# Kernel optimization log

Measured on AMD Instinct MI355X. Metric: run time of the kernel, lower is better.

The kernel has to match this reference:

```python
import jax, jax.numpy as jnp
import numpy as np

B, T, DIM = 2, 2048, 2048
N_HEADS, N_KV_HEADS = 16, 4
HEAD_DIM = DIM // N_HEADS  # 128
N_REP = N_HEADS // N_KV_HEADS  # 4
ROPE_THETA = 10000.0


def setup_inputs() -> dict:
    key = jax.random.key(0)
    ks = jax.random.split(key, 5)
    x = jax.random.normal(ks[0], (B, T, DIM), dtype=jnp.float32)
    # RoPE tables (equivalent to complex freqs_cis = exp(i * t * inv_freq))
    inv_freq = 1.0 / (ROPE_THETA ** (np.arange(0, HEAD_DIM, 2, dtype=np.float32) / HEAD_DIM))
    t = np.arange(T, dtype=np.float32)
    ang = np.outer(t, inv_freq)  # (T, HEAD_DIM//2)
    freqs_cos = jnp.asarray(np.cos(ang), dtype=jnp.float32)
    freqs_sin = jnp.asarray(np.sin(ang), dtype=jnp.float32)
    s = 0.02
    wq = jax.random.normal(ks[1], (DIM, N_HEADS * HEAD_DIM), dtype=jnp.float32) * s
    wk = jax.random.normal(ks[2], (DIM, N_KV_HEADS * HEAD_DIM), dtype=jnp.float32) * s
    wv = jax.random.normal(ks[3], (DIM, N_KV_HEADS * HEAD_DIM), dtype=jnp.float32) * s
    wo = jax.random.normal(ks[4], (N_HEADS * HEAD_DIM, DIM), dtype=jnp.float32) * s
    return {"x": x, "freqs_cos": freqs_cos, "freqs_sin": freqs_sin,
            "wq": wq, "wk": wk, "wv": wv, "wo": wo}


def _apply_rope(t, cos, sin):
    # t: (B, H, T, hd); cos/sin: (T, hd//2); interleaved pairs like view_as_complex
    tr = t[..., 0::2]
    ti = t[..., 1::2]
    c = cos[None, None, :, :]
    s = sin[None, None, :, :]
    out_r = tr * c - ti * s
    out_i = tr * s + ti * c
    return jnp.stack([out_r, out_i], axis=-1).reshape(t.shape)


def reference(x, freqs_cos, freqs_sin, wq, wk, wv, wo):
    Bb, Tt, C = x.shape
    q = (x @ wq).reshape(Bb, Tt, N_HEADS, HEAD_DIM).transpose(0, 2, 1, 3)      # (B,H,T,hd)
    k = (x @ wk).reshape(Bb, Tt, N_KV_HEADS, HEAD_DIM).transpose(0, 2, 1, 3)   # (B,KV,T,hd)
    v = (x @ wv).reshape(Bb, Tt, N_KV_HEADS, HEAD_DIM).transpose(0, 2, 1, 3)
    q = _apply_rope(q, freqs_cos[:Tt], freqs_sin[:Tt])
    k = _apply_rope(k, freqs_cos[:Tt], freqs_sin[:Tt])
    # GQA repeat_kv
    k = jnp.repeat(k, N_REP, axis=1)  # (B,H,T,hd)
    v = jnp.repeat(v, N_REP, axis=1)
    scale = 1.0 / jnp.sqrt(jnp.float32(HEAD_DIM))
    scores = jnp.einsum("bhqd,bhkd->bhqk", q, k) * scale
    causal = jnp.tril(jnp.ones((Tt, Tt), dtype=bool))
    scores = jnp.where(causal[None, None], scores, jnp.float32(-jnp.inf))
    attn = jax.nn.softmax(scores, axis=-1)
    out = jnp.einsum("bhqk,bhkd->bhqd", attn, v)          # (B,H,T,hd)
    out = out.transpose(0, 2, 1, 3).reshape(Bb, Tt, C)
    return out @ wo
```

## Files before the change

### kernel.cpp

```cpp
#include <hip/hip_runtime.h>
#include <hip/hip_bf16.h>

#define SEQT 2048
#define NH 16
#define HD 128

typedef __bf16 bf16;
typedef __bf16 bf16x4 __attribute__((ext_vector_type(4)));
typedef __bf16 bf16x8 __attribute__((ext_vector_type(8)));
typedef float f32x4 __attribute__((ext_vector_type(4)));

__device__ inline void glds16(const bf16* g, bf16* l) {
  __builtin_amdgcn_global_load_lds(
      (const __attribute__((address_space(1))) unsigned int*)g,
      (__attribute__((address_space(3))) unsigned int*)l, 16, 0, 0);
}

__global__ __launch_bounds__(256) void k_convert(const float* __restrict__ in,
                                                 bf16* __restrict__ out, int n8) {
  int i = blockIdx.x * 256 + threadIdx.x;
  if (i >= n8) return;
  const float4* p = (const float4*)in + (size_t)i * 2;
  float4 a = p[0], b = p[1];
  bf16x8 o;
  o[0] = (bf16)a.x; o[1] = (bf16)a.y; o[2] = (bf16)a.z; o[3] = (bf16)a.w;
  o[4] = (bf16)b.x; o[5] = (bf16)b.y; o[6] = (bf16)b.z; o[7] = (bf16)b.w;
  *((bf16x8*)out + i) = o;
}

__global__ __launch_bounds__(256) void k_transpose(const float* __restrict__ in,
                                                   bf16* __restrict__ out, int R, int C) {
  __shared__ float tile[32][33];
  int c0 = blockIdx.x * 32, r0 = blockIdx.y * 32;
  int tx = threadIdx.x, ty = threadIdx.y;
#pragma unroll
  for (int i = 0; i < 4; i++)
    tile[ty + i * 8][tx] = in[(size_t)(r0 + ty + i * 8) * C + c0 + tx];
  __syncthreads();
#pragma unroll
  for (int i = 0; i < 4; i++) {
    int r = ty + i * 8;
    out[(size_t)(c0 + r) * R + r0 + tx] = (bf16)tile[tx][r];
  }
}

template <typename OutT>
__global__ __launch_bounds__(256) void k_gemm(const bf16* __restrict__ A,
                                              const bf16* __restrict__ Bt,
                                              OutT* __restrict__ C,
                                              int M, int N, int K, int ldc) {
  __shared__ bf16 Al[128 * 32];
  __shared__ bf16 Bl[128 * 32];
  int tid = threadIdx.x;
  int m0 = blockIdx.y * 128, n0 = blockIdx.x * 128;
  int wid = tid >> 6, lane = tid & 63;
  int wr = (wid >> 1) * 64, wc = (wid & 1) * 64;
  int lr = lane & 15, lk = (lane >> 4) * 8;
  f32x4 acc[4][4] = {};

  for (int k0 = 0; k0 < K; k0 += 32) {
#pragma unroll
    for (int i = 0; i < 2; i++) {
      int idx = i * 256 + tid;
      int r = idx >> 2, kc = (idx & 3) * 8;
      glds16(A + (size_t)(m0 + r) * K + k0 + kc, Al + idx * 8);
      glds16(Bt + (size_t)(n0 + r) * K + k0 + kc, Bl + idx * 8);
    }
    __syncthreads();
    bf16x8 af[4], bfr[4];
#pragma unroll
    for (int mi = 0; mi < 4; mi++) af[mi] = *(const bf16x8*)&Al[(wr + mi * 16 + lr) * 32 + lk];
#pragma unroll
    for (int ni = 0; ni < 4; ni++) bfr[ni] = *(const bf16x8*)&Bl[(wc + ni * 16 + lr) * 32 + lk];
#pragma unroll
    for (int mi = 0; mi < 4; mi++)
#pragma unroll
      for (int ni = 0; ni < 4; ni++)
        acc[mi][ni] = __builtin_amdgcn_mfma_f32_16x16x32_bf16(af[mi], bfr[ni], acc[mi][ni], 0, 0, 0);
    __syncthreads();
  }

  int rbase = m0 + wr + ((lane >> 4) << 2);
#pragma unroll
  for (int mi = 0; mi < 4; mi++)
#pragma unroll
    for (int ni = 0; ni < 4; ni++)
#pragma unroll
      for (int r = 0; r < 4; r++) {
        int row = rbase + mi * 16 + r;
        int col = n0 + wc + ni * 16 + lr;
        C[(size_t)row * ldc + col] = (OutT)acc[mi][ni][r];
      }
}

__global__ __launch_bounds__(256) void k_rope(bf16* __restrict__ qkv,
                                              const float* __restrict__ fcos,
                                              const float* __restrict__ fsin) {
  int gid = blockIdx.x * 256 + threadIdx.x;
  int row = gid / 1280;
  int p = gid % 1280;
  int head = p >> 6;
  int dp = p & 63;
  int t = row & (SEQT - 1);
  int colbase = head < NH ? head * HD : NH * HD + (head - NH) * HD;
  bf16* ptr = qkv + (size_t)row * 3072 + colbase + dp * 2;
  float a = (float)ptr[0], b = (float)ptr[1];
  float c = fcos[t * 64 + dp], s = fsin[t * 64 + dp];
  ptr[0] = (bf16)(a * c - b * s);
  ptr[1] = (bf16)(a * s + b * c);
}

__global__ __launch_bounds__(256, 2) void k_attn(const bf16* __restrict__ qkv,
                                                 bf16* __restrict__ attout) {
  __shared__ bf16 Kl[2][64 * 128];
  __shared__ bf16 Vt[128][72];
  __shared__ bf16 Pl[4][16][72];
  int bid = blockIdx.x;
  int qt = 31 - (bid >> 5);
  int bh = bid & 31;
  int b = bh >> 4, h = bh & 15, kvh = h >> 2;
  int tid = threadIdx.x, wid = tid >> 6, lane = tid & 63;
  int lr = lane & 15;
  int g = lane >> 4;
  int g4 = g * 4, g8 = g * 8, g16 = g * 16;
  int swz = (lr & 7) << 4;
  int q0 = qt * 64;
  const float scale = 0.08838834764831845f;

  const bf16* kgbase = qkv + (size_t)b * SEQT * 3072 + 2048 + kvh * HD;
  const bf16* vgbase = kgbase + 512;

  bf16x8 qf[4];
  {
    const bf16* qb = qkv + (size_t)(b * SEQT + q0 + wid * 16 + lr) * 3072 + h * HD;
#pragma unroll
    for (int db = 0; db < 4; db++) qf[db] = *(const bf16x8*)(qb + db * 32 + g8);
  }
  float mrun[4] = {-INFINITY, -INFINITY, -INFINITY, -INFINITY};
  float lpart[4] = {0.f, 0.f, 0.f, 0.f};
  f32x4 o[8] = {};
  int nkt = qt + 1;
  int qg0 = q0 + wid * 16 + g4;

  int kq4 = (wid * 4 + g) * 4;
  int dc = lr * 8;
  int xr = (lr & 7) << 3;
  int kvw = kq4 ^ xr;

  bf16x8 vr0, vr1, vr2, vr3;

#pragma unroll
  for (int r = 0; r < 4; r++) {
    int ci = r * 256 + tid;
    int row = ci >> 4;
    int sl = (ci & 15) ^ (row & 7);
    glds16(kgbase + (size_t)row * 3072 + sl * 8, &Kl[0][ci * 8]);
  }
  {
    const bf16* vrow = vgbase + (size_t)kq4 * 3072 + dc;
    vr0 = *(const bf16x8*)(vrow);
    vr1 = *(const bf16x8*)(vrow + 3072);
    vr2 = *(const bf16x8*)(vrow + 6144);
    vr3 = *(const bf16x8*)(vrow + 9216);
  }

  for (int kt = 0; kt < nkt; kt++) {
    int cur = kt & 1;
    asm volatile("s_waitcnt vmcnt(0)" ::: "memory");

#pragma unroll
    for (int j = 0; j < 8; j++) {
      bf16x4 w;
      w[0] = vr0[j]; w[1] = vr1[j]; w[2] = vr2[j]; w[3] = vr3[j];
      *(bf16x4*)&Vt[dc + j][kvw] = w;
    }

    if (kt + 1 < nkt) {
      int kv1 = (kt + 1) * 64;
      bf16* kdst = &Kl[(kt + 1) & 1][0];
#pragma unroll
      for (int r = 0; r < 4; r++) {
        int ci = r * 256 + tid;
        int row = ci >> 4;
        int sl = (ci & 15) ^ (row & 7);
        glds16(kgbase + (size_t)(kv1 + row) * 3072 + sl * 8, kdst + ci * 8);
      }
      const bf16* vrow = vgbase + (size_t)(kv1 + kq4) * 3072 + dc;
      vr0 = *(const bf16x8*)(vrow);
      vr1 = *(const bf16x8*)(vrow + 3072);
      vr2 = *(const bf16x8*)(vrow + 6144);
      vr3 = *(const bf16x8*)(vrow + 9216);
    }

    asm volatile("s_waitcnt lgkmcnt(0)" ::: "memory");
    __builtin_amdgcn_sched_barrier(0);
    __builtin_amdgcn_s_barrier();
    __builtin_amdgcn_sched_barrier(0);

    int kv0 = kt * 64;
    f32x4 s[4] = {};
    __builtin_amdgcn_s_setprio(1);
#pragma unroll
    for (int cb = 0; cb < 4; cb++) {
      const char* krow = (const char*)(&Kl[cur][0] + (cb * 16 + lr) * 128);
#pragma unroll
      for (int db = 0; db < 4; db++) {
        bf16x8 kf = *(const bf16x8*)(krow + ((db * 64 + g16) ^ swz));
        s[cb] = __builtin_amdgcn_mfma_f32_16x16x32_bf16(qf[db], kf, s[cb], 0, 0, 0);
      }
    }
    __builtin_amdgcn_s_setprio(0);

    float pv[4][4];
    float pmax[4] = {-INFINITY, -INFINITY, -INFINITY, -INFINITY};
#pragma unroll
    for (int cb = 0; cb < 4; cb++) {
      int kvg = kv0 + cb * 16 + lr;
#pragma unroll
      for (int r = 0; r < 4; r++) {
        float v = s[cb][r] * scale;
        if (kvg > qg0 + r) v = -INFINITY;
        pv[cb][r] = v;
        pmax[r] = fmaxf(pmax[r], v);
      }
    }
#pragma unroll
    for (int mk = 1; mk <= 8; mk <<= 1)
#pragma unroll
      for (int r = 0; r < 4; r++) pmax[r] = fmaxf(pmax[r], __shfl_xor(pmax[r], mk));
    float grow = fmaxf(fmaxf(pmax[0] - mrun[0], pmax[1] - mrun[1]),
                       fmaxf(pmax[2] - mrun[2], pmax[3] - mrun[3]));
    if (!__all(grow <= 8.0f)) {
#pragma unroll
      for (int r = 0; r < 4; r++) {
        float mnew = fmaxf(mrun[r], pmax[r]);
        float alpha = __expf(mrun[r] - mnew);
        mrun[r] = mnew;
        lpart[r] *= alpha;
#pragma unroll
        for (int df = 0; df < 8; df++) o[df][r] *= alpha;
      }
    }
#pragma unroll
    for (int r = 0; r < 4; r++) {
      float rs = 0.f;
#pragma unroll
      for (int cb = 0; cb < 4; cb++) {
        float e = __expf(pv[cb][r] - mrun[r]);
        pv[cb][r] = e;
        rs += e;
      }
      lpart[r] += rs;
    }

#pragma unroll
    for (int cb = 0; cb < 4; cb++)
#pragma unroll
      for (int r = 0; r < 4; r++)
        Pl[wid][g4 + r][cb * 16 + lr] = (bf16)pv[cb][r];

    __builtin_amdgcn_s_setprio(1);
#pragma unroll
    for (int kb = 0; kb < 2; kb++) {
      bf16x8 pa = *(const bf16x8*)&Pl[wid][lr][kb * 32 + g8];
#pragma unroll
      for (int df = 0; df < 8; df++) {
        int d = df * 16 + lr;
        int xv = ((d >> 3) & 7) << 3;
        bf16x8 vb = *(const bf16x8*)&Vt[d][(kb * 32 + g8) ^ xv];
        o[df] = __builtin_amdgcn_mfma_f32_16x16x32_bf16(pa, vb, o[df], 0, 0, 0);
      }
    }
    __builtin_amdgcn_s_setprio(0);
    __builtin_amdgcn_sched_barrier(0);
    __builtin_amdgcn_s_barrier();
    __builtin_amdgcn_sched_barrier(0);
  }

#pragma unroll
  for (int mk = 1; mk <= 8; mk <<= 1)
#pragma unroll
    for (int r = 0; r < 4; r++) lpart[r] += __shfl_xor(lpart[r], mk);
#pragma unroll
  for (int r = 0; r < 4; r++) {
    float inv = 1.f / lpart[r];
    int qg = q0 + wid * 16 + g4 + r;
    bf16* ob = attout + (size_t)(b * SEQT + qg) * 2048 + h * HD;
#pragma unroll
    for (int df = 0; df < 8; df++)
      ob[df * 16 + lr] = (bf16)(o[df][r] * inv);
  }
}

extern "C" void kernel_launch(void* const* d_in, const int* in_sizes, int n_in,
                              void* d_out, int out_size, void* d_ws, size_t ws_size,
                              hipStream_t stream) {
  const float* x    = (const float*)d_in[0];
  const float* fcos = (const float*)d_in[1];
  const float* fsin = (const float*)d_in[2];
  const float* wq   = (const float*)d_in[3];
  const float* wk   = (const float*)d_in[4];
  const float* wv   = (const float*)d_in[5];
  const float* wo   = (const float*)d_in[6];
  float* out = (float*)d_out;

  char* ws = (char*)d_ws;
  bf16* XB  = (bf16*)ws;
  bf16* W   = (bf16*)(ws + 16777216);
  bf16* QKV = (bf16*)(ws + 16777216 + 12582912);

  dim3 tb(32, 8);
  k_transpose<<<dim3(64, 64), tb, 0, stream>>>(wq, W, 2048, 2048);
  k_transpose<<<dim3(16, 64), tb, 0, stream>>>(wk, W + 2048 * 2048, 2048, 512);
  k_transpose<<<dim3(16, 64), tb, 0, stream>>>(wv, W + 2560 * 2048, 2048, 512);
  k_convert<<<4096, 256, 0, stream>>>(x, XB, 1048576);
  k_gemm<bf16><<<dim3(24, 32), 256, 0, stream>>>(XB, W, QKV, 4096, 3072, 2048, 3072);
  k_rope<<<20480, 256, 0, stream>>>(QKV, fcos, fsin);
  k_attn<<<1024, 256, 0, stream>>>(QKV, XB);
  k_transpose<<<dim3(64, 64), tb, 0, stream>>>(wo, W, 2048, 2048);
  k_gemm<float><<<dim3(16, 32), 256, 0, stream>>>(XB, W, out, 4096, 2048, 2048, 2048);
}
```

Measured before the change: 242.2 us.

## Restructure attention to 32x32 MFMA with 128-row query tiles and register-resident P

```diff
diff --git a/kernel.cpp b/kernel.cpp
--- a/kernel.cpp
+++ b/kernel.cpp
@@ -9,11 +9,18 @@
 typedef __bf16 bf16x4 __attribute__((ext_vector_type(4)));
 typedef __bf16 bf16x8 __attribute__((ext_vector_type(8)));
 typedef float f32x4 __attribute__((ext_vector_type(4)));
+typedef float f32x16 __attribute__((ext_vector_type(16)));
 
 __device__ inline void glds16(const bf16* g, bf16* l) {
   __builtin_amdgcn_global_load_lds(
       (const __attribute__((address_space(1))) unsigned int*)g,
       (__attribute__((address_space(3))) unsigned int*)l, 16, 0, 0);
+}
+
+__device__ inline unsigned int cvtpk(float a, float b) {
+  unsigned int d;
+  asm("v_cvt_pk_bf16_f32 %0, %1, %2" : "=v"(d) : "v"(a), "v"(b));
+  return d;
 }
 
 __global__ __launch_bounds__(256) void k_convert(const float* __restrict__ in,
@@ -114,34 +121,34 @@
                                                  bf16* __restrict__ attout) {
   __shared__ bf16 Kl[2][64 * 128];
   __shared__ bf16 Vt[128][72];
-  __shared__ bf16 Pl[4][16][72];
+  __shared__ float Atab[4][32];
   int bid = blockIdx.x;
-  int qt = 31 - (bid >> 5);
+  int qt = 15 - (bid >> 5);
   int bh = bid & 31;
   int b = bh >> 4, h = bh & 15, kvh = h >> 2;
   int tid = threadIdx.x, wid = tid >> 6, lane = tid & 63;
-  int lr = lane & 15;
-  int g = lane >> 4;
-  int g4 = g * 4, g8 = g * 8, g16 = g * 16;
-  int swz = (lr & 7) << 4;
-  int q0 = qt * 64;
-  const float scale = 0.08838834764831845f;
+  int li = lane & 31, hi = lane >> 5;
+  int q0 = qt * 128;
+  int qmin = q0 + wid * 32, qmax = qmin + 31;
+  int qlane = qmin + li;
+  const float C1 = 0.12751744979927212f;
 
   const bf16* kgbase = qkv + (size_t)b * SEQT * 3072 + 2048 + kvh * HD;
   const bf16* vgbase = kgbase + 512;
 
-  bf16x8 qf[4];
+  bf16x8 qf[8];
   {
-    const bf16* qb = qkv + (size_t)(b * SEQT + q0 + wid * 16 + lr) * 3072 + h * HD;
-#pragma unroll
-    for (int db = 0; db < 4; db++) qf[db] = *(const bf16x8*)(qb + db * 32 + g8);
-  }
-  float mrun[4] = {-INFINITY, -INFINITY, -INFINITY, -INFINITY};
-  float lpart[4] = {0.f, 0.f, 0.f, 0.f};
-  f32x4 o[8] = {};
-  int nkt = qt + 1;
-  int qg0 = q0 + wid * 16 + g4;
-
+    const bf16* qb = qkv + (size_t)(b * SEQT + qlane) * 3072 + h * HD + hi * 8;
+#pragma unroll
+    for (int ks = 0; ks < 8; ks++) qf[ks] = *(const bf16x8*)(qb + ks * 16);
+  }
+
+  float mrun = -INFINITY, lpart = 0.f;
+  f32x16 o0 = {}, o1 = {}, o2 = {}, o3 = {};
+  int nkt = 2 * qt + 2;
+
+  int g = (lane >> 4) & 3;
+  int lr = lane & 15;
   int kq4 = (wid * 4 + g) * 4;
   int dc = lr * 8;
   int xr = (lr & 7) << 3;
@@ -153,7 +160,7 @@
   for (int r = 0; r < 4; r++) {
     int ci = r * 256 + tid;
     int row = ci >> 4;
-    int sl = (ci & 15) ^ (row & 7);
+    int sl = (ci & 15) ^ (row & 15);
     glds16(kgbase + (size_t)row * 3072 + sl * 8, &Kl[0][ci * 8]);
   }
   {
@@ -166,6 +173,7 @@
 
   for (int kt = 0; kt < nkt; kt++) {
     int cur = kt & 1;
+    int kv0 = kt * 64;
     asm volatile("s_waitcnt vmcnt(0)" ::: "memory");
 
 #pragma unroll
@@ -176,13 +184,13 @@
     }
 
     if (kt + 1 < nkt) {
-      int kv1 = (kt + 1) * 64;
-      bf16* kdst = &Kl[(kt + 1) & 1][0];
+      int kv1 = kv0 + 64;
+      bf16* kdst = &Kl[cur ^ 1][0];
 #pragma unroll
       for (int r = 0; r < 4; r++) {
         int ci = r * 256 + tid;
         int row = ci >> 4;
-        int sl = (ci & 15) ^ (row & 7);
+        int sl = (ci & 15) ^ (row & 15);
         glds16(kgbase + (size_t)(kv1 + row) * 3072 + sl * 8, kdst + ci * 8);
       }
       const bf16* vrow = vgbase + (size_t)(kv1 + kq4) * 3072 + dc;
@@ -197,98 +205,145 @@
     __builtin_amdgcn_s_barrier();
     __builtin_amdgcn_sched_barrier(0);
 
-    int kv0 = kt * 64;
-    f32x4 s[4] = {};
-    __builtin_amdgcn_s_setprio(1);
-#pragma unroll
-    for (int cb = 0; cb < 4; cb++) {
-      const char* krow = (const char*)(&Kl[cur][0] + (cb * 16 + lr) * 128);
-#pragma unroll
-      for (int db = 0; db < 4; db++) {
-        bf16x8 kf = *(const bf16x8*)(krow + ((db * 64 + g16) ^ swz));
-        s[cb] = __builtin_amdgcn_mfma_f32_16x16x32_bf16(qf[db], kf, s[cb], 0, 0, 0);
-      }
+    if (kv0 <= qmax) {
+      f32x16 s0 = {}, s1 = {};
+      const char* kb0 = (const char*)&Kl[cur][0] + li * 256;
+      __builtin_amdgcn_s_setprio(1);
+#pragma unroll
+      for (int ks = 0; ks < 8; ks++) {
+        int off = ((ks * 2 + hi) ^ (li & 15)) << 4;
+        bf16x8 kf0 = *(const bf16x8*)(kb0 + off);
+        bf16x8 kf1 = *(const bf16x8*)(kb0 + 8192 + off);
+        s0 = __builtin_amdgcn_mfma_f32_32x32x16_bf16(kf0, qf[ks], s0, 0, 0, 0);
+        s1 = __builtin_amdgcn_mfma_f32_32x32x16_bf16(kf1, qf[ks], s1, 0, 0, 0);
+      }
+      __builtin_amdgcn_s_setprio(0);
+
+      if (kv0 + 63 > qmin) {
+        int base0 = kv0 + 4 * hi - qlane;
+#pragma unroll
+        for (int r = 0; r < 16; r++) {
+          int off = (r & 3) + 8 * (r >> 2);
+          if (base0 + off > 0) s0[r] = -INFINITY;
+          if (base0 + 32 + off > 0) s1[r] = -INFINITY;
+        }
+      }
+
+      float pm = s0[0];
+#pragma unroll
+      for (int r = 1; r < 16; r++) pm = fmaxf(pm, s0[r]);
+#pragma unroll
+      for (int r = 0; r < 16; r++) pm = fmaxf(pm, s1[r]);
+      pm = fmaxf(pm, __shfl_xor(pm, 32));
+
+      if (!__all(pm - mrun <= 62.0f)) {
+        float mnew = fmaxf(mrun, pm);
+        float alpha = exp2f((mrun - mnew) * C1);
+        mrun = mnew;
+        lpart *= alpha;
+        Atab[wid][li] = alpha;
+        asm volatile("s_waitcnt lgkmcnt(0)" ::: "memory");
+        f32x4 a0 = *(const f32x4*)&Atab[wid][4 * hi];
+        f32x4 a1 = *(const f32x4*)&Atab[wid][4 * hi + 8];
+        f32x4 a2 = *(const f32x4*)&Atab[wid][4 * hi + 16];
+        f32x4 a3 = *(const f32x4*)&Atab[wid][4 * hi + 24];
+#define RESC_RR(rr, av)                                            \
+  _Pragma("unroll") for (int i = 0; i < 4; i++) {                  \
+    float f = av[i];                                               \
+    o0[rr * 4 + i] *= f; o1[rr * 4 + i] *= f;                      \
+    o2[rr * 4 + i] *= f; o3[rr * 4 + i] *= f;                      \
+  }
+        RESC_RR(0, a0) RESC_RR(1, a1) RESC_RR(2, a2) RESC_RR(3, a3)
+#undef RESC_RR
+      }
+
+      float mC = mrun * C1;
+      float rs = 0.f;
+#pragma unroll
+      for (int r = 0; r < 16; r++) {
+        float p = exp2f(fmaf(s0[r], C1, -mC));
+        s0[r] = p; rs += p;
+      }
+#pragma unroll
+      for (int r = 0; r < 16; r++) {
+        float p = exp2f(fmaf(s1[r], C1, -mC));
+        s1[r] = p; rs += p;
+      }
+      lpart += rs;
+
+      union U4 { unsigned int u[4]; bf16x8 v; };
+      U4 pa0, pa1, pa2, pa3;
+      {
+        unsigned int e0 = cvtpk(s0[0], s0[1]), e1 = cvtpk(s0[2], s0[3]);
+        unsigned int e2 = cvtpk(s0[4], s0[5]), e3 = cvtpk(s0[6], s0[7]);
+        unsigned int e4 = cvtpk(s0[8], s0[9]), e5 = cvtpk(s0[10], s0[11]);
+        unsigned int e6 = cvtpk(s0[12], s0[13]), e7 = cvtpk(s0[14], s0[15]);
+        unsigned int t0 = __shfl_xor(e0, 32), t1 = __shfl_xor(e1, 32);
+        unsigned int t2 = __shfl_xor(e2, 32), t3 = __shfl_xor(e3, 32);
+        unsigned int t4 = __shfl_xor(e4, 32), t5 = __shfl_xor(e5, 32);
+        unsigned int t6 = __shfl_xor(e6, 32), t7 = __shfl_xor(e7, 32);
+        pa0.u[0] = hi ? t2 : e0;  pa0.u[1] = hi ? t3 : e1;
+        pa0.u[2] = hi ? e2 : t0;  pa0.u[3] = hi ? e3 : t1;
+        pa1.u[0] = hi ? t6 : e4;  pa1.u[1] = hi ? t7 : e5;
+        pa1.u[2] = hi ? e6 : t4;  pa1.u[3] = hi ? e7 : t5;
+        unsigned int f0 = cvtpk(s1[0], s1[1]), f1 = cvtpk(s1[2], s1[3]);
+        unsigned int f2 = cvtpk(s1[4], s1[5]), f3 = cvtpk(s1[6], s1[7]);
+        unsigned int f4 = cvtpk(s1[8], s1[9]), f5 = cvtpk(s1[10], s1[11]);
+        unsigned int f6 = cvtpk(s1[12], s1[13]), f7 = cvtpk(s1[14], s1[15]);
+        unsigned int u0 = __shfl_xor(f0, 32), u1 = __shfl_xor(f1, 32);
+        unsigned int u2 = __shfl_xor(f2, 32), u3 = __shfl_xor(f3, 32);
+        unsigned int u4 = __shfl_xor(f4, 32), u5 = __shfl_xor(f5, 32);
+        unsigned int u6 = __shfl_xor(f6, 32), u7 = __shfl_xor(f7, 32);
+        pa2.u[0] = hi ? u2 : f0;  pa2.u[1] = hi ? u3 : f1;
+        pa2.u[2] = hi ? f2 : u0;  pa2.u[3] = hi ? f3 : u1;
+        pa3.u[0] = hi ? u6 : f4;  pa3.u[1] = hi ? u7 : f5;
+        pa3.u[2] = hi ? f6 : u4;  pa3.u[3] = hi ? f7 : u5;
+      }
+
+      __builtin_amdgcn_s_setprio(1);
+#define PV_DB(OACC, DB)                                                      \
+  {                                                                          \
+    int d = DB * 32 + li;                                                    \
+    int xv = ((d >> 3) & 7) << 3;                                            \
+    bf16x8 vb0 = *(const bf16x8*)&Vt[d][(hi * 8) ^ xv];                      \
+    bf16x8 vb1 = *(const bf16x8*)&Vt[d][(16 + hi * 8) ^ xv];                 \
+    bf16x8 vb2 = *(const bf16x8*)&Vt[d][(32 + hi * 8) ^ xv];                 \
+    bf16x8 vb3 = *(const bf16x8*)&Vt[d][(48 + hi * 8) ^ xv];                 \
+    OACC = __builtin_amdgcn_mfma_f32_32x32x16_bf16(pa0.v, vb0, OACC, 0, 0, 0); \
+    OACC = __builtin_amdgcn_mfma_f32_32x32x16_bf16(pa1.v, vb1, OACC, 0, 0, 0); \
+    OACC = __builtin_amdgcn_mfma_f32_32x32x16_bf16(pa2.v, vb2, OACC, 0, 0, 0); \
+    OACC = __builtin_amdgcn_mfma_f32_32x32x16_bf16(pa3.v, vb3, OACC, 0, 0, 0); \
+  }
+      PV_DB(o0, 0) PV_DB(o1, 1) PV_DB(o2, 2) PV_DB(o3, 3)
+#undef PV_DB
+      __builtin_amdgcn_s_setprio(0);
     }
-    __builtin_amdgcn_s_setprio(0);
-
-    float pv[4][4];
-    float pmax[4] = {-INFINITY, -INFINITY, -INFINITY, -INFINITY};
-#pragma unroll
-    for (int cb = 0; cb < 4; cb++) {
-      int kvg = kv0 + cb * 16 + lr;
-#pragma unroll
-      for (int r = 0; r < 4; r++) {
-        float v = s[cb][r] * scale;
-        if (kvg > qg0 + r) v = -INFINITY;
-        pv[cb][r] = v;
-        pmax[r] = fmaxf(pmax[r], v);
-      }
-    }
-#pragma unroll
-    for (int mk = 1; mk <= 8; mk <<= 1)
-#pragma unroll
-      for (int r = 0; r < 4; r++) pmax[r] = fmaxf(pmax[r], __shfl_xor(pmax[r], mk));
-    float grow = fmaxf(fmaxf(pmax[0] - mrun[0], pmax[1] - mrun[1]),
-                       fmaxf(pmax[2] - mrun[2], pmax[3] - mrun[3]));
-    if (!__all(grow <= 8.0f)) {
-#pragma unroll
-      for (int r = 0; r < 4; r++) {
-        float mnew = fmaxf(mrun[r], pmax[r]);
-        float alpha = __expf(mrun[r] - mnew);
-        mrun[r] = mnew;
-        lpart[r] *= alpha;
-#pragma unroll
-        for (int df = 0; df < 8; df++) o[df][r] *= alpha;
-      }
-    }
-#pragma unroll
-    for (int r = 0; r < 4; r++) {
-      float rs = 0.f;
-#pragma unroll
-      for (int cb = 0; cb < 4; cb++) {
-        float e = __expf(pv[cb][r] - mrun[r]);
-        pv[cb][r] = e;
-        rs += e;
-      }
-      lpart[r] += rs;
-    }
-
-#pragma unroll
-    for (int cb = 0; cb < 4; cb++)
-#pragma unroll
-      for (int r = 0; r < 4; r++)
-        Pl[wid][g4 + r][cb * 16 + lr] = (bf16)pv[cb][r];
-
-    __builtin_amdgcn_s_setprio(1);
-#pragma unroll
-    for (int kb = 0; kb < 2; kb++) {
-      bf16x8 pa = *(const bf16x8*)&Pl[wid][lr][kb * 32 + g8];
-#pragma unroll
-      for (int df = 0; df < 8; df++) {
-        int d = df * 16 + lr;
-        int xv = ((d >> 3) & 7) << 3;
-        bf16x8 vb = *(const bf16x8*)&Vt[d][(kb * 32 + g8) ^ xv];
-        o[df] = __builtin_amdgcn_mfma_f32_16x16x32_bf16(pa, vb, o[df], 0, 0, 0);
-      }
-    }
-    __builtin_amdgcn_s_setprio(0);
+
     __builtin_amdgcn_sched_barrier(0);
     __builtin_amdgcn_s_barrier();
     __builtin_amdgcn_sched_barrier(0);
   }
 
-#pragma unroll
-  for (int mk = 1; mk <= 8; mk <<= 1)
-#pragma unroll
-    for (int r = 0; r < 4; r++) lpart[r] += __shfl_xor(lpart[r], mk);
-#pragma unroll
-  for (int r = 0; r < 4; r++) {
-    float inv = 1.f / lpart[r];
-    int qg = q0 + wid * 16 + g4 + r;
-    bf16* ob = attout + (size_t)(b * SEQT + qg) * 2048 + h * HD;
-#pragma unroll
-    for (int df = 0; df < 8; df++)
-      ob[df * 16 + lr] = (bf16)(o[df][r] * inv);
+  lpart += __shfl_xor(lpart, 32);
+  Atab[wid][li] = 1.f / lpart;
+  asm volatile("s_waitcnt lgkmcnt(0)" ::: "memory");
+  f32x4 l0 = *(const f32x4*)&Atab[wid][4 * hi];
+  f32x4 l1 = *(const f32x4*)&Atab[wid][4 * hi + 8];
+  f32x4 l2 = *(const f32x4*)&Atab[wid][4 * hi + 16];
+  f32x4 l3 = *(const f32x4*)&Atab[wid][4 * hi + 24];
+  {
+    size_t obase = (size_t)(b * SEQT) * 2048 + h * HD;
+#define STORE_RR(rr, lv)                                                     \
+  _Pragma("unroll") for (int i = 0; i < 4; i++) {                            \
+    int q = qmin + 4 * hi + 8 * rr + i;                                      \
+    size_t rowb = obase + (size_t)q * 2048 + li;                             \
+    attout[rowb + 0]  = (bf16)(o0[rr * 4 + i] * lv[i]);                      \
+    attout[rowb + 32] = (bf16)(o1[rr * 4 + i] * lv[i]);                      \
+    attout[rowb + 64] = (bf16)(o2[rr * 4 + i] * lv[i]);                      \
+    attout[rowb + 96] = (bf16)(o3[rr * 4 + i] * lv[i]);                      \
+  }
+    STORE_RR(0, l0) STORE_RR(1, l1) STORE_RR(2, l2) STORE_RR(3, l3)
+#undef STORE_RR
   }
 }
 
@@ -316,7 +371,7 @@
   k_convert<<<4096, 256, 0, stream>>>(x, XB, 1048576);
   k_gemm<bf16><<<dim3(24, 32), 256, 0, stream>>>(XB, W, QKV, 4096, 3072, 2048, 3072);
   k_rope<<<20480, 256, 0, stream>>>(QKV, fcos, fsin);
-  k_attn<<<1024, 256, 0, stream>>>(QKV, XB);
+  k_attn<<<512, 256, 0, stream>>>(QKV, XB);
   k_transpose<<<dim3(64, 64), tb, 0, stream>>>(wo, W, 2048, 2048);
   k_gemm<float><<<dim3(16, 32), 256, 0, stream>>>(XB, W, out, 4096, 2048, 2048, 2048);
 }
```

New measurement: 241.6 us. No clear change (-0.3%).
